# Kernel optimization log

Hardware: AMD Instinct MI355X
Metric: run time of the kernel (lower is better)

## Reference

```python
import jax, jax.numpy as jnp
import numpy as np

B, S, H, E, V, T = 512, 140, 512, 256, 1000, 21  # T = day_walk_max + 1
PAD, SOS = 0, 2
NDAYS, DLEN = 7, 20


def setup_inputs() -> dict:
    key = jax.random.key(0)
    ks = jax.random.split(key, 16)
    s = 0.05
    return {
        "encoder_hidden": jax.random.normal(ks[0], (1, B, H), jnp.float32),
        "encoder_outputs": jax.random.normal(ks[1], (B, S, H), jnp.float32),
        "label": jax.random.randint(ks[2], (B, T + 1), 0, V),
        "numpairs": jax.random.randint(ks[3], (B, S), 0, 10),
        "emb": jax.random.normal(ks[4], (V, E), jnp.float32) * s,
        "W_ih": jax.random.normal(ks[5], (3 * H, E), jnp.float32) * s,
        "W_hh": jax.random.normal(ks[6], (3 * H, H), jnp.float32) * s,
        "b_ih": jnp.zeros((3 * H,), jnp.float32),
        "b_hh": jnp.zeros((3 * H,), jnp.float32),
        "attn_Wa": jax.random.normal(ks[7], (H, H), jnp.float32) * s,
        "wa_W": jax.random.normal(ks[8], (H, 2 * H), jnp.float32) * s,
        "fc_W": jax.random.normal(ks[9], (V, H), jnp.float32) * s,
        "fc_b": jnp.zeros((V,), jnp.float32),
    }


def _decode(encoder_hidden, encoder_outputs, label, numpairs,
            emb, W_ih, W_hh, b_ih, b_hh, attn_Wa, wa_W, fc_W, fc_b):
    # Luong 'general' attention over 7 day-segments of 20 steps each.
    enc_days = encoder_outputs.reshape(B, NDAYS, DLEN, H)
    mask_day = numpairs.reshape(B, NDAYS, DLEN) != PAD
    # energy is hidden-independent: precompute once  [B,7,20,H]
    energy_day = jnp.einsum('bdsh,gh->bdsg', enc_days, attn_Wa)

    def step(carry, lab_t):
        dec_in, h = carry  # dec_in [B] int, h [B,H]
        # per-day additive attention with numpair padding mask
        sc = jnp.einsum('bh,bdsh->bds', h, energy_day)
        sc = jnp.where(mask_day, sc, jnp.float32(-1e9))
        wd = jax.nn.softmax(sc, axis=-1)
        week = jnp.einsum('bds,bdsh->bdh', wd, enc_days)  # [B,7,H]
        # GRU cell (PyTorch gate layout r,z,n); dropout is identity at eval
        x = emb[dec_in]  # [B,E]
        gi = x @ W_ih.T + b_ih
        gh = h @ W_hh.T + b_hh
        i_r, i_z, i_n = jnp.split(gi, 3, axis=-1)
        h_r, h_z, h_n = jnp.split(gh, 3, axis=-1)
        r = jax.nn.sigmoid(i_r + h_r)
        z = jax.nn.sigmoid(i_z + h_z)
        n = jnp.tanh(i_n + r * h_n)
        h_new = (1.0 - z) * n + z * h  # [B,H]
        # week-level attention over the 7 day contexts (no mask)
        ew = jnp.einsum('bdh,gh->bdg', week, attn_Wa)
        aw = jax.nn.softmax(jnp.einsum('bh,bdh->bd', h_new, ew), axis=-1)
        ctx = jnp.einsum('bd,bdh->bh', aw, week)
        concat = jnp.concatenate([h_new, ctx], axis=-1)  # [B,2H]
        out = jax.nn.log_softmax(jnp.tanh(concat @ wa_W.T) @ fc_W.T + fc_b, axis=-1)
        return (lab_t, h_new), out  # teacher forcing: next input = label[:, t]

    dec0 = jnp.full((B,), SOS, dtype=label.dtype)
    h0 = encoder_hidden[0]  # [B,H]
    labels_t = label[:, :T].T  # [T,B]
    (last_in, _), outs = jax.lax.scan(step, (dec0, h0), labels_t)
    decoder_outputs = jnp.transpose(outs, (1, 0, 2))  # [B,T,V]
    return decoder_outputs, last_in[:, None]


def reference(encoder_hidden, encoder_outputs, label, numpairs,
              emb, W_ih, W_hh, b_ih, b_hh, attn_Wa, wa_W, fc_W, fc_b):
    return _decode(encoder_hidden, encoder_outputs, label, numpairs,
                   emb, W_ih, W_hh, b_ih, b_hh, attn_Wa, wa_W, fc_W, fc_b)
```

## Files before the change

kernel.cpp:

```cpp
#include <hip/hip_runtime.h>
#include <math.h>

typedef __attribute__((ext_vector_type(8))) short bf16x8;
typedef __attribute__((ext_vector_type(4))) float f32x4;

constexpr int NB = 512;
constexpr int NS = 140;
constexpr int NH = 512;
constexpr int NE = 256;
constexpr int NV = 1000;
constexpr int NVP = 1024;
constexpr int NT = 21;
constexpr int ND = 7;
constexpr int DL = 20;
constexpr int SOS = 2;
constexpr int LSTR = NT + 1;
constexpr int NROW = NT * NB;

__device__ __forceinline__ unsigned short f2bf(float f) {
  union { float f; unsigned u; } v; v.f = f;
  unsigned r = v.u + 0x7fffu + ((v.u >> 16) & 1u);
  return (unsigned short)(r >> 16);
}
__device__ __forceinline__ float bf2f(unsigned short h) {
  union { unsigned u; float f; } v; v.u = ((unsigned)h) << 16;
  return v.f;
}
__device__ __forceinline__ void unp8(uint4 v, float* o) {
  o[0] = bf2f((unsigned short)(v.x & 0xffffu)); o[1] = bf2f((unsigned short)(v.x >> 16));
  o[2] = bf2f((unsigned short)(v.y & 0xffffu)); o[3] = bf2f((unsigned short)(v.y >> 16));
  o[4] = bf2f((unsigned short)(v.z & 0xffffu)); o[5] = bf2f((unsigned short)(v.z >> 16));
  o[6] = bf2f((unsigned short)(v.w & 0xffffu)); o[7] = bf2f((unsigned short)(v.w >> 16));
}

template<int A16, int EPI, int OUT16>
__device__ __forceinline__ void gemm_body(
    const float* __restrict__ Af, const unsigned short* __restrict__ Ah,
    const unsigned short* __restrict__ Bt, const float* __restrict__ bias,
    float* __restrict__ C, unsigned short* __restrict__ C16,
    int K, int lda, int ldc, int bx, int by,
    unsigned short* As, unsigned short* Bs)
{
  const int tid = threadIdx.x;
  const int rowBase = by * 64, colBase = bx * 64;
  const int wave = tid >> 6, lane = tid & 63, quad = lane >> 4, l15 = lane & 15;
  const int rw = (wave & 1) * 32, cw = (wave >> 1) * 32;

  f32x4 acc[2][2];
#pragma unroll
  for (int i = 0; i < 2; ++i)
#pragma unroll
    for (int j = 0; j < 2; ++j)
#pragma unroll
      for (int r = 0; r < 4; ++r) acc[i][j][r] = 0.f;

  const int ar = tid >> 2;
  const int kq = (tid & 3) * 8;
  const float* aptrf = nullptr;
  const unsigned short* aptrh = nullptr;
  if (A16) aptrh = Ah + (size_t)(rowBase + ar) * lda + kq;
  else     aptrf = Af + (size_t)(rowBase + ar) * lda + kq;
  const unsigned short* bptr = Bt + (size_t)(colBase + ar) * K + kq;
  unsigned short* asd = &As[ar * 40 + kq];
  unsigned short* bsd = &Bs[ar * 40 + kq];

  float4 x0, x1;
  uint4 av;
  if (A16) {
    av = *(const uint4*)aptrh;
  } else {
    x0 = *(const float4*)aptrf; x1 = *(const float4*)(aptrf + 4);
  }
  uint4 bv = *(const uint4*)bptr;

  int cur = 0;
  for (int k0 = 0; k0 < K; k0 += 32) {
    uint4 aw;
    if (A16) {
      aw = av;
    } else {
      aw.x = (unsigned)f2bf(x0.x) | ((unsigned)f2bf(x0.y) << 16);
      aw.y = (unsigned)f2bf(x0.z) | ((unsigned)f2bf(x0.w) << 16);
      aw.z = (unsigned)f2bf(x1.x) | ((unsigned)f2bf(x1.y) << 16);
      aw.w = (unsigned)f2bf(x1.z) | ((unsigned)f2bf(x1.w) << 16);
    }
    *(uint4*)(asd + cur * 2560) = aw;
    *(uint4*)(bsd + cur * 2560) = bv;

    const int kn = k0 + 32;
    if (kn < K) {
      if (A16) {
        av = *(const uint4*)(aptrh + kn);
      } else {
        x0 = *(const float4*)(aptrf + kn);
        x1 = *(const float4*)(aptrf + kn + 4);
      }
      bv = *(const uint4*)(bptr + kn);
    }
    __syncthreads();

    const unsigned short* Ab = As + cur * 2560;
    const unsigned short* Bb = Bs + cur * 2560;
    const bf16x8 af0 = *(const bf16x8*)&Ab[(rw + l15) * 40 + quad * 8];
    const bf16x8 af1 = *(const bf16x8*)&Ab[(rw + 16 + l15) * 40 + quad * 8];
    const bf16x8 bf0 = *(const bf16x8*)&Bb[(cw + l15) * 40 + quad * 8];
    const bf16x8 bf1 = *(const bf16x8*)&Bb[(cw + 16 + l15) * 40 + quad * 8];
    acc[0][0] = __builtin_amdgcn_mfma_f32_16x16x32_bf16(af0, bf0, acc[0][0], 0, 0, 0);
    acc[0][1] = __builtin_amdgcn_mfma_f32_16x16x32_bf16(af0, bf1, acc[0][1], 0, 0, 0);
    acc[1][0] = __builtin_amdgcn_mfma_f32_16x16x32_bf16(af1, bf0, acc[1][0], 0, 0, 0);
    acc[1][1] = __builtin_amdgcn_mfma_f32_16x16x32_bf16(af1, bf1, acc[1][1], 0, 0, 0);
    cur ^= 1;
  }

#pragma unroll
  for (int i = 0; i < 2; ++i) {
    const int grow = rowBase + rw + 16 * i + quad * 4;
#pragma unroll
    for (int j = 0; j < 2; ++j) {
      const int gcol = colBase + cw + 16 * j + l15;
#pragma unroll
      for (int r = 0; r < 4; ++r) {
        float vo = acc[i][j][r];
        if (EPI == 1) vo += (gcol < NV) ? bias[gcol] : 0.f;
        if (EPI == 2) vo = tanhf(vo);
        if (OUT16) C16[(size_t)(grow + r) * ldc + gcol] = f2bf(vo);
        else       C[(size_t)(grow + r) * ldc + gcol] = vo;
      }
    }
  }
}

template<int A16, int EPI, int OUT16>
__global__ __launch_bounds__(256) void gemm_k(
    const float* __restrict__ Af, const unsigned short* __restrict__ Ah,
    const unsigned short* __restrict__ Bt, const float* __restrict__ bias,
    float* __restrict__ C, unsigned short* __restrict__ C16,
    int K, int lda, int ldc)
{
  __shared__ unsigned short As[2 * 64 * 40];
  __shared__ unsigned short Bs[2 * 64 * 40];
  gemm_body<A16, EPI, OUT16>(Af, Ah, Bt, bias, C, C16, K, lda, ldc,
                             blockIdx.x, blockIdx.y, As, Bs);
}

__global__ __launch_bounds__(256) void gemm_gather(
    const float* __restrict__ emb, const unsigned short* __restrict__ Wiht,
    unsigned short* __restrict__ Gi, const int* __restrict__ label)
{
  __shared__ unsigned short As[64 * 40];
  __shared__ unsigned short Bs[64 * 40];
  const int tid = threadIdx.x;
  const int rowBase = blockIdx.y * 64, colBase = blockIdx.x * 64;
  const int wave = tid >> 6, lane = tid & 63, quad = lane >> 4, l15 = lane & 15;
  const int rw = (wave & 1) * 32, cw = (wave >> 1) * 32;
  const int K = 256;

  f32x4 acc[2][2];
#pragma unroll
  for (int i = 0; i < 2; ++i)
#pragma unroll
    for (int j = 0; j < 2; ++j)
#pragma unroll
      for (int r = 0; r < 4; ++r) acc[i][j][r] = 0.f;

  const int ar = tid >> 2;
  const int kq = (tid & 3) * 8;
  const int aRowG = rowBase + ar;
  const int t = aRowG >> 9;
  const int b = aRowG & 511;
  const int dec = (t == 0) ? SOS : label[b * LSTR + (t - 1)];
  const float* aptr = emb + (size_t)dec * NE + kq;
  const unsigned short* bptr = Wiht + (size_t)(colBase + ar) * K + kq;
  unsigned short* asd = &As[ar * 40 + kq];
  unsigned short* bsd = &Bs[ar * 40 + kq];

  float4 x0 = *(const float4*)aptr;
  float4 x1 = *(const float4*)(aptr + 4);
  uint4 bv = *(const uint4*)bptr;

  for (int k0 = 0; k0 < K; k0 += 32) {
    uint4 aw;
    aw.x = (unsigned)f2bf(x0.x) | ((unsigned)f2bf(x0.y) << 16);
    aw.y = (unsigned)f2bf(x0.z) | ((unsigned)f2bf(x0.w) << 16);
    aw.z = (unsigned)f2bf(x1.x) | ((unsigned)f2bf(x1.y) << 16);
    aw.w = (unsigned)f2bf(x1.z) | ((unsigned)f2bf(x1.w) << 16);
    *(uint4*)asd = aw;
    *(uint4*)bsd = bv;
    __syncthreads();
    const int kn = k0 + 32;
    if (kn < K) {
      x0 = *(const float4*)(aptr + kn);
      x1 = *(const float4*)(aptr + kn + 4);
      bv = *(const uint4*)(bptr + kn);
    }
    const bf16x8 af0 = *(const bf16x8*)&As[(rw + l15) * 40 + quad * 8];
    const bf16x8 af1 = *(const bf16x8*)&As[(rw + 16 + l15) * 40 + quad * 8];
    const bf16x8 bf0 = *(const bf16x8*)&Bs[(cw + l15) * 40 + quad * 8];
    const bf16x8 bf1 = *(const bf16x8*)&Bs[(cw + 16 + l15) * 40 + quad * 8];
    acc[0][0] = __builtin_amdgcn_mfma_f32_16x16x32_bf16(af0, bf0, acc[0][0], 0, 0, 0);
    acc[0][1] = __builtin_amdgcn_mfma_f32_16x16x32_bf16(af0, bf1, acc[0][1], 0, 0, 0);
    acc[1][0] = __builtin_amdgcn_mfma_f32_16x16x32_bf16(af1, bf0, acc[1][0], 0, 0, 0);
    acc[1][1] = __builtin_amdgcn_mfma_f32_16x16x32_bf16(af1, bf1, acc[1][1], 0, 0, 0);
    __syncthreads();
  }

#pragma unroll
  for (int i = 0; i < 2; ++i) {
    const int grow = rowBase + rw + 16 * i + quad * 4;
#pragma unroll
    for (int j = 0; j < 2; ++j) {
      const int gcol = colBase + cw + 16 * j + l15;
#pragma unroll
      for (int r = 0; r < 4; ++r)
        Gi[(size_t)(grow + r) * 1536 + gcol] = f2bf(acc[i][j][r]);
    }
  }
}

__global__ __launch_bounds__(256) void step_fused(
    const float* __restrict__ Ht, const unsigned short* __restrict__ W1pk,
    const unsigned short* __restrict__ Gi_t,
    const float* __restrict__ b_ih, const float* __restrict__ b_hh,
    float* __restrict__ Hnext, float* __restrict__ Ut,
    unsigned short* __restrict__ U16t, int notLast)
{
  __shared__ __align__(16) char smem[46080];
  unsigned short* As = (unsigned short*)smem;
  unsigned short* Bs = (unsigned short*)(smem + 5120);
  float* Gbuf = (float*)smem;

  const int tid = threadIdx.x;
  const int wave = tid >> 6, lane = tid & 63, quad = lane >> 4, l15 = lane & 15;
  const int rowBase = blockIdx.y * 32;
  const int colBase = blockIdx.x * 256;

  f32x4 acc[2][4];
#pragma unroll
  for (int i = 0; i < 2; ++i)
#pragma unroll
    for (int j = 0; j < 4; ++j)
#pragma unroll
      for (int r = 0; r < 4; ++r) acc[i][j][r] = 0.f;

  const int ar = tid >> 3;
  const int kqa = (tid & 7) * 4;
  const float* aptr = Ht + (size_t)(rowBase + ar) * NH + kqa;
  const unsigned short* bbase = W1pk + (size_t)(colBase + tid) * 32;
  unsigned short* asd = As + ar * 40 + kqa;
  unsigned short* bsd = Bs + tid * 40;

  float4 xa = *(const float4*)aptr;
  uint4 bv0 = *(const uint4*)(bbase + 0);
  uint4 bv1 = *(const uint4*)(bbase + 8);
  uint4 bv2 = *(const uint4*)(bbase + 16);
  uint4 bv3 = *(const uint4*)(bbase + 24);

  int cur = 0;
  for (int k0 = 0; k0 < NH; k0 += 32) {
    ushort4 aw;
    aw.x = f2bf(xa.x); aw.y = f2bf(xa.y); aw.z = f2bf(xa.z); aw.w = f2bf(xa.w);
    *(ushort4*)(asd + cur * 1280) = aw;
    *(uint4*)(bsd + cur * 10240 + 0)  = bv0;
    *(uint4*)(bsd + cur * 10240 + 8)  = bv1;
    *(uint4*)(bsd + cur * 10240 + 16) = bv2;
    *(uint4*)(bsd + cur * 10240 + 24) = bv3;

    const int kn = k0 + 32;
    if (kn < NH) {
      xa = *(const float4*)(aptr + kn);
      const unsigned short* nb = bbase + (size_t)(kn >> 5) * (2048 * 32);
      bv0 = *(const uint4*)(nb + 0);
      bv1 = *(const uint4*)(nb + 8);
      bv2 = *(const uint4*)(nb + 16);
      bv3 = *(const uint4*)(nb + 24);
    }
    __syncthreads();

    const unsigned short* Ab = As + cur * 1280;
    const unsigned short* Bb = Bs + cur * 10240;
    const bf16x8 af0 = *(const bf16x8*)&Ab[(l15) * 40 + quad * 8];
    const bf16x8 af1 = *(const bf16x8*)&Ab[(16 + l15) * 40 + quad * 8];
#pragma unroll
    for (int j = 0; j < 4; ++j) {
      const bf16x8 bf = *(const bf16x8*)&Bb[(wave * 64 + j * 16 + l15) * 40 + quad * 8];
      acc[0][j] = __builtin_amdgcn_mfma_f32_16x16x32_bf16(af0, bf, acc[0][j], 0, 0, 0);
      acc[1][j] = __builtin_amdgcn_mfma_f32_16x16x32_bf16(af1, bf, acc[1][j], 0, 0, 0);
    }
    cur ^= 1;
  }
  __syncthreads();

#pragma unroll
  for (int i = 0; i < 2; ++i) {
#pragma unroll
    for (int j = 0; j < 4; ++j) {
#pragma unroll
      for (int r = 0; r < 4; ++r) {
        const int rl = 16 * i + quad * 4 + r;
        const int col = j * 16 + l15;
        if (wave == 3) {
          const float v = acc[i][j][r];
          const size_t off = (size_t)(rowBase + rl) * NH + blockIdx.x * 64 + col;
          Ut[off] = v;
          U16t[off] = f2bf(v);
        } else {
          Gbuf[(wave * 32 + rl) * 72 + col] = acc[i][j][r];
        }
      }
    }
  }
  __syncthreads();

  if (notLast) {
    const int rl = tid >> 3, c8 = (tid & 7) * 8;
    const int bg = rowBase + rl;
    const int jg = blockIdx.x * 64 + c8;
    const float* g0 = Gbuf + (0 * 32 + rl) * 72 + c8;
    const float* g1 = Gbuf + (1 * 32 + rl) * 72 + c8;
    const float* g2 = Gbuf + (2 * 32 + rl) * 72 + c8;
    const unsigned short* gp = Gi_t + (size_t)bg * 1536;
    float gr[8], gz[8], gn[8];
    { uint4 a = *(const uint4*)(gp + jg);        unp8(a, gr); }
    { uint4 a = *(const uint4*)(gp + 512 + jg);  unp8(a, gz); }
    { uint4 a = *(const uint4*)(gp + 1024 + jg); unp8(a, gn); }
    const float* hR = Ht + (size_t)bg * NH + jg;
    float* hW = Hnext + (size_t)bg * NH + jg;
    const float4 ho0 = *(const float4*)hR;
    const float4 ho1 = *(const float4*)(hR + 4);
    const float hov[8] = {ho0.x, ho0.y, ho0.z, ho0.w, ho1.x, ho1.y, ho1.z, ho1.w};
    float o[8];
#pragma unroll
    for (int c = 0; c < 8; ++c) {
      const int j = jg + c;
      const float ir  = gr[c] + b_ih[j];
      const float iz  = gz[c] + b_ih[512 + j];
      const float inn = gn[c] + b_ih[1024 + j];
      const float hr  = g0[c] + b_hh[j];
      const float hz  = g1[c] + b_hh[512 + j];
      const float hn  = g2[c] + b_hh[1024 + j];
      const float rg = 1.f / (1.f + expf(-(ir + hr)));
      const float zg = 1.f / (1.f + expf(-(iz + hz)));
      const float ng = tanhf(inn + rg * hn);
      o[c] = (1.f - zg) * ng + zg * hov[c];
    }
    *(float4*)hW = make_float4(o[0], o[1], o[2], o[3]);
    *(float4*)(hW + 4) = make_float4(o[4], o[5], o[6], o[7]);
  }
}

__global__ __launch_bounds__(256) void day_attn_mfma(
    const float* __restrict__ enc, const int* __restrict__ numpairs,
    const unsigned short* __restrict__ U16, unsigned short* __restrict__ week)
{
  __shared__ unsigned short Erow[32 * 520];
  __shared__ unsigned short ETs[512 * 36];
  __shared__ float S_lds[32 * 33];
  __shared__ unsigned short P_lds[32 * 40];

  const int tid = threadIdx.x;
  const int wave = tid >> 6, lane = tid & 63;
  const int quad = lane >> 4, l15 = lane & 15;
  const int b = blockIdx.x / ND, d = blockIdx.x % ND;
  const int mt = wave >> 1, nt = wave & 1;

  for (int i = tid; i < 512 * 6; i += 256)
    *(unsigned*)&ETs[(i / 6) * 36 + 20 + (i % 6) * 2] = 0;
  for (int i = tid; i < 640; i += 256) ((unsigned*)P_lds)[i] = 0;

  const float* eb = enc + ((size_t)b * NS + d * DL) * NH;
  for (int f = tid; f < DL * NH / 4; f += 256) {
    const int s = f >> 7, h = (f & 127) * 4;
    const float4 v = *(const float4*)(eb + s * NH + h);
    ushort4 hs;
    hs.x = f2bf(v.x); hs.y = f2bf(v.y); hs.z = f2bf(v.z); hs.w = f2bf(v.w);
    *(ushort4*)&Erow[s * 520 + h] = hs;
  }

  bf16x8 qa[16];
  {
    const int m = mt * 16 + l15;
    const int t = (m < NT + 1) ? m : NT;
    const unsigned short* qp = U16 + ((size_t)t * NB + b) * NH + quad * 8;
#pragma unroll
    for (int ks = 0; ks < 16; ++ks)
      qa[ks] = *(const bf16x8*)(qp + ks * 32);
  }
  __syncthreads();

  for (int i = tid; i < 64 * DL; i += 256) {
    const int s = i % DL, h8 = i / DL;
    const uint4 v = *(const uint4*)&Erow[s * 520 + h8 * 8];
    const unsigned short* u = (const unsigned short*)&v;
#pragma unroll
    for (int c = 0; c < 8; ++c)
      ETs[(h8 * 8 + c) * 36 + s] = u[c];
  }

  f32x4 sacc = {0.f, 0.f, 0.f, 0.f};
#pragma unroll
  for (int ks = 0; ks < 16; ++ks) {
    const bf16x8 bf = *(const bf16x8*)&Erow[(nt * 16 + l15) * 520 + ks * 32 + quad * 8];
    sacc = __builtin_amdgcn_mfma_f32_16x16x32_bf16(qa[ks], bf, sacc, 0, 0, 0);
  }
#pragma unroll
  for (int r = 0; r < 4; ++r)
    S_lds[(mt * 16 + quad * 4 + r) * 33 + nt * 16 + l15] = sacc[r];
  __syncthreads();

  {
    const int r = tid >> 3, c = tid & 7;
    const int base = b * NS + d * DL;
    float v0 = S_lds[r * 33 + c];
    if (numpairs[base + c] == 0) v0 = -1e9f;
    float v1 = S_lds[r * 33 + c + 8];
    if (numpairs[base + c + 8] == 0) v1 = -1e9f;
    float v2 = -1e30f;
    if (c < 4) {
      v2 = S_lds[r * 33 + c + 16];
      if (numpairs[base + c + 16] == 0) v2 = -1e9f;
    }
    float mx = fmaxf(fmaxf(v0, v1), v2);
    mx = fmaxf(mx, __shfl_xor(mx, 1));
    mx = fmaxf(mx, __shfl_xor(mx, 2));
    mx = fmaxf(mx, __shfl_xor(mx, 4));
    const float e0 = expf(v0 - mx), e1 = expf(v1 - mx);
    const float e2 = (c < 4) ? expf(v2 - mx) : 0.f;
    float sm = e0 + e1 + e2;
    sm += __shfl_xor(sm, 1);
    sm += __shfl_xor(sm, 2);
    sm += __shfl_xor(sm, 4);
    const float inv = 1.f / sm;
    P_lds[r * 40 + c] = f2bf(e0 * inv);
    P_lds[r * 40 + c + 8] = f2bf(e1 * inv);
    if (c < 4) P_lds[r * 40 + c + 16] = f2bf(e2 * inv);
  }
  __syncthreads();

  const bf16x8 pa = *(const bf16x8*)&P_lds[(mt * 16 + l15) * 40 + quad * 8];
#pragma unroll
  for (int j = 0; j < 16; ++j) {
    const int hcol = nt * 256 + j * 16;
    const bf16x8 bf = *(const bf16x8*)&ETs[(hcol + l15) * 36 + quad * 8];
    f32x4 oacc = {0.f, 0.f, 0.f, 0.f};
    oacc = __builtin_amdgcn_mfma_f32_16x16x32_bf16(pa, bf, oacc, 0, 0, 0);
#pragma unroll
    for (int r = 0; r < 4; ++r) {
      const int t = mt * 16 + quad * 4 + r;
      if (t < NT)
        week[(((size_t)t * NB + b) * ND + d) * NH + hcol + l15] = f2bf(oacc[r]);
    }
  }
}

__global__ __launch_bounds__(256) void wk_ctx(
    const float* __restrict__ U, const unsigned short* __restrict__ week,
    const float* __restrict__ H, unsigned short* __restrict__ concat)
{
  __shared__ float scS[16 * ND];
  __shared__ float awS[16 * ND];
  const int tid = threadIdx.x;
  const int t = blockIdx.x >> 5;
  const int grp = blockIdx.x & 31;
  const int b16 = tid >> 4, k16 = tid & 15;
  const int b = grp * 16 + b16;
  const float* vp = U + ((size_t)(t + 1) * NB + b) * NH + k16 * 32;
  const size_t wrow = ((size_t)t * NB + b) * ND;

  for (int d = 0; d < ND; ++d) {
    const unsigned short* wp = week + (wrow + d) * NH + k16 * 32;
    float p = 0.f;
#pragma unroll
    for (int q = 0; q < 8; ++q) {
      const float4 a = *(const float4*)(vp + q * 4);
      const ushort4 wv = *(const ushort4*)(wp + q * 4);
      p += a.x * bf2f(wv.x) + a.y * bf2f(wv.y) + a.z * bf2f(wv.z) + a.w * bf2f(wv.w);
    }
    p += __shfl_down(p, 8); p += __shfl_down(p, 4);
    p += __shfl_down(p, 2); p += __shfl_down(p, 1);
    if (k16 == 0) scS[b16 * ND + d] = p;
  }
  __syncthreads();
  if (tid < 16) {
    float s[ND], mx = -1e30f;
    for (int d = 0; d < ND; ++d) { s[d] = scS[tid * ND + d]; mx = fmaxf(mx, s[d]); }
    float sum = 0.f;
    for (int d = 0; d < ND; ++d) { float e = expf(s[d] - mx); s[d] = e; sum += e; }
    const float inv = 1.f / sum;
    for (int d = 0; d < ND; ++d) awS[tid * ND + d] = s[d] * inv;
  }
  __syncthreads();

  const int c0 = k16 * 32;
  const float* hp = H + ((size_t)(t + 1) * NB + b) * NH + c0;
  float aw[ND];
#pragma unroll
  for (int d = 0; d < ND; ++d) aw[d] = awS[b16 * ND + d];
  unsigned short* crow = concat + ((size_t)t * NB + b) * 1024;
#pragma unroll
  for (int q = 0; q < 8; ++q) {
    const int c = c0 + q * 4;
    const float4 hv = *(const float4*)(hp + q * 4);
    ushort4 hs;
    hs.x = f2bf(hv.x); hs.y = f2bf(hv.y); hs.z = f2bf(hv.z); hs.w = f2bf(hv.w);
    *(ushort4*)(crow + c) = hs;
    float4 cv = make_float4(0.f, 0.f, 0.f, 0.f);
#pragma unroll
    for (int d = 0; d < ND; ++d) {
      const ushort4 wv = *(const ushort4*)(week + (wrow + d) * NH + c);
      cv.x += aw[d] * bf2f(wv.x); cv.y += aw[d] * bf2f(wv.y);
      cv.z += aw[d] * bf2f(wv.z); cv.w += aw[d] * bf2f(wv.w);
    }
    ushort4 cs;
    cs.x = f2bf(cv.x); cs.y = f2bf(cv.y); cs.z = f2bf(cv.z); cs.w = f2bf(cv.w);
    *(ushort4*)(crow + 512 + c) = cs;
  }
}

__global__ __launch_bounds__(256) void lsm_k(
    const float* __restrict__ logits, float* __restrict__ out)
{
  __shared__ float red[8];
  const int tid = threadIdx.x;
  const int wave = tid >> 6, lane = tid & 63;
  const int r = blockIdx.x;
  const int t = r >> 9, b = r & (NB - 1);
  const float* row = logits + (size_t)r * NVP;
  float v[4];
  float mx = -1e30f;
#pragma unroll
  for (int k = 0; k < 4; ++k) {
    const int c = tid + k * 256;
    v[k] = row[c];
    if (c < NV) mx = fmaxf(mx, v[k]);
  }
#pragma unroll
  for (int off = 32; off; off >>= 1) mx = fmaxf(mx, __shfl_xor(mx, off));
  if (lane == 0) red[wave] = mx;
  __syncthreads();
  mx = fmaxf(fmaxf(red[0], red[1]), fmaxf(red[2], red[3]));
  float s = 0.f;
#pragma unroll
  for (int k = 0; k < 4; ++k) {
    const int c = tid + k * 256;
    if (c < NV) s += expf(v[k] - mx);
  }
#pragma unroll
  for (int off = 32; off; off >>= 1) s += __shfl_xor(s, off);
  if (lane == 0) red[4 + wave] = s;
  __syncthreads();
  const float lse = mx + logf(red[4] + red[5] + red[6] + red[7]);
  float* orow = out + ((size_t)b * NT + t) * NV;
#pragma unroll
  for (int k = 0; k < 4; ++k) {
    const int c = tid + k * 256;
    if (c < NV) orow[c] = v[k] - lse;
  }
}

__global__ void write_last(const int* __restrict__ label, float* __restrict__ out2)
{
  const int b = blockIdx.x * 256 + threadIdx.x;
  if (b < NB) out2[b] = (float)label[b * LSTR + (NT - 1)];
}

__global__ __launch_bounds__(256) void pack_w1pk(
    const float* __restrict__ Whh, const float* __restrict__ Wa,
    unsigned short* __restrict__ W1pk)
{
  const int idx = blockIdx.x * 256 + threadIdx.x;
  const int np = idx >> 9, k = idx & 511;
  const int g = np >> 8, rem = np & 255, gate = rem >> 6, j = g * 64 + (rem & 63);
  float v;
  if (gate < 3) v = Whh[(size_t)(gate * 512 + j) * 512 + k];
  else          v = Wa[(size_t)k * 512 + j];
  W1pk[((size_t)(k >> 5) * 2048 + np) * 32 + (k & 31)] = f2bf(v);
}

__global__ __launch_bounds__(256) void cast4(
    const float4* __restrict__ in, ushort4* __restrict__ out, int n4)
{
  const int i = blockIdx.x * 256 + threadIdx.x;
  if (i < n4) {
    const float4 x = in[i];
    ushort4 r;
    r.x = f2bf(x.x); r.y = f2bf(x.y); r.z = f2bf(x.z); r.w = f2bf(x.w);
    out[i] = r;
  }
}

extern "C" void kernel_launch(void* const* d_in, const int* in_sizes, int n_in,
                              void* d_out, int out_size, void* d_ws, size_t ws_size,
                              hipStream_t stream)
{
  const float* enc_h  = (const float*)d_in[0];
  const float* enc    = (const float*)d_in[1];
  const int*   label  = (const int*)d_in[2];
  const int*   numprs = (const int*)d_in[3];
  const float* emb    = (const float*)d_in[4];
  const float* W_ih   = (const float*)d_in[5];
  const float* W_hh   = (const float*)d_in[6];
  const float* b_ih   = (const float*)d_in[7];
  const float* b_hh   = (const float*)d_in[8];
  const float* Wa     = (const float*)d_in[9];
  const float* wa_W   = (const float*)d_in[10];
  const float* fc_W   = (const float*)d_in[11];
  const float* fc_b   = (const float*)d_in[12];
  float* out = (float*)d_out;

  float* f = (float*)d_ws;
  float* H_all   = f; f += (size_t)(NT + 1) * NB * NH;
  float* U_all   = f; f += (size_t)(NT + 1) * NB * NH;
  float* logitsW = f; f += (size_t)NROW * NVP;
  unsigned short* us = (unsigned short*)f;
  unsigned short* U16    = us; us += (size_t)(NT + 1) * NB * NH;
  unsigned short* W1pk   = us; us += (size_t)2048 * 512;
  unsigned short* W3t    = us; us += (size_t)512 * 1024;
  unsigned short* W4t    = us; us += (size_t)NVP * 512;
  unsigned short* Wiht   = us; us += (size_t)1536 * 256;
  unsigned short* Gi     = us; us += (size_t)NT * NB * 1536;
  unsigned short* week   = us; us += (size_t)NT * NB * ND * NH;
  unsigned short* concatW= us; us += (size_t)NROW * 1024;
  unsigned short* aBuf   = us; us += (size_t)NROW * 512;

  const dim3 blk(256);
  const size_t BH = (size_t)NB * NH;

  hipMemcpyAsync(H_all, enc_h, BH * sizeof(float),
                 hipMemcpyDeviceToDevice, stream);

  pack_w1pk<<<dim3(2048 * 512 / 256), blk, 0, stream>>>(W_hh, Wa, W1pk);
  cast4<<<dim3(512 * 1024 / 4 / 256), blk, 0, stream>>>(
      (const float4*)wa_W, (ushort4*)W3t, 512 * 1024 / 4);
  cast4<<<dim3((NV * 512 / 4 + 255) / 256), blk, 0, stream>>>(
      (const float4*)fc_W, (ushort4*)W4t, NV * 512 / 4);
  hipMemsetAsync(W4t + (size_t)NV * 512, 0, (size_t)(NVP - NV) * 512 * 2, stream);
  cast4<<<dim3(1536 * 256 / 4 / 256), blk, 0, stream>>>(
      (const float4*)W_ih, (ushort4*)Wiht, 1536 * 256 / 4);
  gemm_gather<<<dim3(24, NT * 8), blk, 0, stream>>>(emb, Wiht, Gi, label);

  for (int t = 0; t <= NT; ++t) {
    const int notLast = (t < NT) ? 1 : 0;
    const int tg = (t < NT) ? t : NT - 1;
    step_fused<<<dim3(8, 16), blk, 0, stream>>>(
        H_all + (size_t)t * BH, W1pk, Gi + (size_t)tg * NB * 1536,
        b_ih, b_hh,
        H_all + (size_t)(notLast ? t + 1 : t) * BH,
        U_all + (size_t)t * BH, U16 + (size_t)t * BH, notLast);
  }

  day_attn_mfma<<<dim3(NB * ND), blk, 0, stream>>>(enc, numprs, U16, week);
  wk_ctx<<<dim3(NT * 32), blk, 0, stream>>>(U_all, week, H_all, concatW);
  gemm_k<1, 2, 1><<<dim3(8, NROW / 64), blk, 0, stream>>>(
      nullptr, concatW, W3t, nullptr, nullptr, aBuf, 1024, 1024, 512);
  gemm_k<1, 1, 0><<<dim3(16, NROW / 64), blk, 0, stream>>>(
      nullptr, aBuf, W4t, fc_b, logitsW, nullptr, 512, 512, NVP);
  lsm_k<<<dim3(NROW), blk, 0, stream>>>(logitsW, out);
  write_last<<<dim3(2), blk, 0, stream>>>(label, out + (size_t)NB * NT * NV);
}
```

Before: 784.8 us.

## Halve step kernel column tile to double grid, shrink day-attention LDS

The per-timestep fused GRU/U kernel now handles 32 hidden columns per block instead of 64, doubling the grid from 128 to 256 blocks and halving per-block LDS and accumulators. The weight packing is changed to match the new gate grouping. Separately, the day-attention kernel transposes the encoder tile in two halves so its transposed buffer needs half the LDS, which should allow more resident blocks at the cost of an extra barrier and a second transpose pass. Each step block now reloads A (hidden state) tiles for fewer output columns, so A traffic doubles.

New measurement: 675.0 us. 14.0% less time.

```diff
diff --git a/kernel.cpp b/kernel.cpp
--- a/kernel.cpp
+++ b/kernel.cpp
@@ -31,6 +31,10 @@
   o[2] = bf2f((unsigned short)(v.y & 0xffffu)); o[3] = bf2f((unsigned short)(v.y >> 16));
   o[4] = bf2f((unsigned short)(v.z & 0xffffu)); o[5] = bf2f((unsigned short)(v.z >> 16));
   o[6] = bf2f((unsigned short)(v.w & 0xffffu)); o[7] = bf2f((unsigned short)(v.w >> 16));
+}
+__device__ __forceinline__ void unp4(uint2 v, float* o) {
+  o[0] = bf2f((unsigned short)(v.x & 0xffffu)); o[1] = bf2f((unsigned short)(v.x >> 16));
+  o[2] = bf2f((unsigned short)(v.y & 0xffffu)); o[3] = bf2f((unsigned short)(v.y >> 16));
 }
 
 template<int A16, int EPI, int OUT16>
@@ -218,13 +222,13 @@
 }
 
 __global__ __launch_bounds__(256) void step_fused(
-    const float* __restrict__ Ht, const unsigned short* __restrict__ W1pk,
+    const float* __restrict__ Ht, const unsigned short* __restrict__ W2,
     const unsigned short* __restrict__ Gi_t,
     const float* __restrict__ b_ih, const float* __restrict__ b_hh,
     float* __restrict__ Hnext, float* __restrict__ Ut,
     unsigned short* __restrict__ U16t, int notLast)
 {
-  __shared__ __align__(16) char smem[46080];
+  __shared__ __align__(16) char smem[25600];
   unsigned short* As = (unsigned short*)smem;
   unsigned short* Bs = (unsigned short*)(smem + 5120);
   float* Gbuf = (float*)smem;
@@ -232,57 +236,51 @@
   const int tid = threadIdx.x;
   const int wave = tid >> 6, lane = tid & 63, quad = lane >> 4, l15 = lane & 15;
   const int rowBase = blockIdx.y * 32;
-  const int colBase = blockIdx.x * 256;
-
-  f32x4 acc[2][4];
+  const int G = blockIdx.x;
+
+  f32x4 acc[2][2];
 #pragma unroll
   for (int i = 0; i < 2; ++i)
 #pragma unroll
-    for (int j = 0; j < 4; ++j)
+    for (int j = 0; j < 2; ++j)
 #pragma unroll
       for (int r = 0; r < 4; ++r) acc[i][j][r] = 0.f;
 
   const int ar = tid >> 3;
   const int kqa = (tid & 7) * 4;
   const float* aptr = Ht + (size_t)(rowBase + ar) * NH + kqa;
-  const unsigned short* bbase = W1pk + (size_t)(colBase + tid) * 32;
+  const unsigned short* bsrc = W2 + (size_t)(G * 128) * 32 + (tid >> 1) * 32 + (tid & 1) * 16;
   unsigned short* asd = As + ar * 40 + kqa;
-  unsigned short* bsd = Bs + tid * 40;
+  unsigned short* bdst = Bs + (tid >> 1) * 40 + (tid & 1) * 16;
 
   float4 xa = *(const float4*)aptr;
-  uint4 bv0 = *(const uint4*)(bbase + 0);
-  uint4 bv1 = *(const uint4*)(bbase + 8);
-  uint4 bv2 = *(const uint4*)(bbase + 16);
-  uint4 bv3 = *(const uint4*)(bbase + 24);
+  uint4 b0 = ((const uint4*)bsrc)[0];
+  uint4 b1 = ((const uint4*)bsrc)[1];
 
   int cur = 0;
-  for (int k0 = 0; k0 < NH; k0 += 32) {
+  for (int c = 0; c < 16; ++c) {
     ushort4 aw;
     aw.x = f2bf(xa.x); aw.y = f2bf(xa.y); aw.z = f2bf(xa.z); aw.w = f2bf(xa.w);
     *(ushort4*)(asd + cur * 1280) = aw;
-    *(uint4*)(bsd + cur * 10240 + 0)  = bv0;
-    *(uint4*)(bsd + cur * 10240 + 8)  = bv1;
-    *(uint4*)(bsd + cur * 10240 + 16) = bv2;
-    *(uint4*)(bsd + cur * 10240 + 24) = bv3;
-
-    const int kn = k0 + 32;
-    if (kn < NH) {
-      xa = *(const float4*)(aptr + kn);
-      const unsigned short* nb = bbase + (size_t)(kn >> 5) * (2048 * 32);
-      bv0 = *(const uint4*)(nb + 0);
-      bv1 = *(const uint4*)(nb + 8);
-      bv2 = *(const uint4*)(nb + 16);
-      bv3 = *(const uint4*)(nb + 24);
+    *(uint4*)(bdst + cur * 5120) = b0;
+    *(uint4*)(bdst + cur * 5120 + 8) = b1;
+
+    const int cn = c + 1;
+    if (cn < 16) {
+      xa = *(const float4*)(aptr + cn * 32);
+      const unsigned short* nb = bsrc + (size_t)cn * (2048 * 32);
+      b0 = ((const uint4*)nb)[0];
+      b1 = ((const uint4*)nb)[1];
     }
     __syncthreads();
 
     const unsigned short* Ab = As + cur * 1280;
-    const unsigned short* Bb = Bs + cur * 10240;
+    const unsigned short* Bb = Bs + cur * 5120;
     const bf16x8 af0 = *(const bf16x8*)&Ab[(l15) * 40 + quad * 8];
     const bf16x8 af1 = *(const bf16x8*)&Ab[(16 + l15) * 40 + quad * 8];
 #pragma unroll
-    for (int j = 0; j < 4; ++j) {
-      const bf16x8 bf = *(const bf16x8*)&Bb[(wave * 64 + j * 16 + l15) * 40 + quad * 8];
+    for (int j = 0; j < 2; ++j) {
+      const bf16x8 bf = *(const bf16x8*)&Bb[(wave * 32 + j * 16 + l15) * 40 + quad * 8];
       acc[0][j] = __builtin_amdgcn_mfma_f32_16x16x32_bf16(af0, bf, acc[0][j], 0, 0, 0);
       acc[1][j] = __builtin_amdgcn_mfma_f32_16x16x32_bf16(af1, bf, acc[1][j], 0, 0, 0);
     }
@@ -293,18 +291,18 @@
 #pragma unroll
   for (int i = 0; i < 2; ++i) {
 #pragma unroll
-    for (int j = 0; j < 4; ++j) {
+    for (int j = 0; j < 2; ++j) {
 #pragma unroll
       for (int r = 0; r < 4; ++r) {
         const int rl = 16 * i + quad * 4 + r;
-        const int col = j * 16 + l15;
+        const int jj = j * 16 + l15;
+        const float v = acc[i][j][r];
         if (wave == 3) {
-          const float v = acc[i][j][r];
-          const size_t off = (size_t)(rowBase + rl) * NH + blockIdx.x * 64 + col;
+          const size_t off = (size_t)(rowBase + rl) * NH + G * 32 + jj;
           Ut[off] = v;
           U16t[off] = f2bf(v);
         } else {
-          Gbuf[(wave * 32 + rl) * 72 + col] = acc[i][j][r];
+          Gbuf[(wave * 32 + rl) * 40 + jj] = v;
         }
       }
     }
@@ -312,39 +310,43 @@
   __syncthreads();
 
   if (notLast) {
-    const int rl = tid >> 3, c8 = (tid & 7) * 8;
+    const int rl = tid >> 3, c4 = (tid & 7) * 4;
     const int bg = rowBase + rl;
-    const int jg = blockIdx.x * 64 + c8;
-    const float* g0 = Gbuf + (0 * 32 + rl) * 72 + c8;
-    const float* g1 = Gbuf + (1 * 32 + rl) * 72 + c8;
-    const float* g2 = Gbuf + (2 * 32 + rl) * 72 + c8;
+    const int j0 = G * 32 + c4;
+    const float4 g0 = *(const float4*)(Gbuf + (0 * 32 + rl) * 40 + c4);
+    const float4 g1 = *(const float4*)(Gbuf + (1 * 32 + rl) * 40 + c4);
+    const float4 g2 = *(const float4*)(Gbuf + (2 * 32 + rl) * 40 + c4);
     const unsigned short* gp = Gi_t + (size_t)bg * 1536;
-    float gr[8], gz[8], gn[8];
-    { uint4 a = *(const uint4*)(gp + jg);        unp8(a, gr); }
-    { uint4 a = *(const uint4*)(gp + 512 + jg);  unp8(a, gz); }
-    { uint4 a = *(const uint4*)(gp + 1024 + jg); unp8(a, gn); }
-    const float* hR = Ht + (size_t)bg * NH + jg;
-    float* hW = Hnext + (size_t)bg * NH + jg;
-    const float4 ho0 = *(const float4*)hR;
-    const float4 ho1 = *(const float4*)(hR + 4);
-    const float hov[8] = {ho0.x, ho0.y, ho0.z, ho0.w, ho1.x, ho1.y, ho1.z, ho1.w};
-    float o[8];
-#pragma unroll
-    for (int c = 0; c < 8; ++c) {
-      const int j = jg + c;
-      const float ir  = gr[c] + b_ih[j];
-      const float iz  = gz[c] + b_ih[512 + j];
-      const float inn = gn[c] + b_ih[1024 + j];
-      const float hr  = g0[c] + b_hh[j];
-      const float hz  = g1[c] + b_hh[512 + j];
-      const float hn  = g2[c] + b_hh[1024 + j];
-      const float rg = 1.f / (1.f + expf(-(ir + hr)));
-      const float zg = 1.f / (1.f + expf(-(iz + hz)));
-      const float ng = tanhf(inn + rg * hn);
+    float gr[4], gz[4], gn[4];
+    { uint2 a = *(const uint2*)(gp + j0);        unp4(a, gr); }
+    { uint2 a = *(const uint2*)(gp + 512 + j0);  unp4(a, gz); }
+    { uint2 a = *(const uint2*)(gp + 1024 + j0); unp4(a, gn); }
+    const float4 bi0 = *(const float4*)(b_ih + j0);
+    const float4 bi1 = *(const float4*)(b_ih + 512 + j0);
+    const float4 bi2 = *(const float4*)(b_ih + 1024 + j0);
+    const float4 bh0 = *(const float4*)(b_hh + j0);
+    const float4 bh1 = *(const float4*)(b_hh + 512 + j0);
+    const float4 bh2 = *(const float4*)(b_hh + 1024 + j0);
+    const float4 ho = *(const float4*)(Ht + (size_t)bg * NH + j0);
+    const float ghr[4] = {g0.x, g0.y, g0.z, g0.w};
+    const float ghz[4] = {g1.x, g1.y, g1.z, g1.w};
+    const float ghn[4] = {g2.x, g2.y, g2.z, g2.w};
+    const float bi0a[4] = {bi0.x, bi0.y, bi0.z, bi0.w};
+    const float bi1a[4] = {bi1.x, bi1.y, bi1.z, bi1.w};
+    const float bi2a[4] = {bi2.x, bi2.y, bi2.z, bi2.w};
+    const float bh0a[4] = {bh0.x, bh0.y, bh0.z, bh0.w};
+    const float bh1a[4] = {bh1.x, bh1.y, bh1.z, bh1.w};
+    const float bh2a[4] = {bh2.x, bh2.y, bh2.z, bh2.w};
+    const float hov[4] = {ho.x, ho.y, ho.z, ho.w};
+    float o[4];
+#pragma unroll
+    for (int c = 0; c < 4; ++c) {
+      const float rg = 1.f / (1.f + expf(-(gr[c] + bi0a[c] + ghr[c] + bh0a[c])));
+      const float zg = 1.f / (1.f + expf(-(gz[c] + bi1a[c] + ghz[c] + bh1a[c])));
+      const float ng = tanhf(gn[c] + bi2a[c] + rg * (ghn[c] + bh2a[c]));
       o[c] = (1.f - zg) * ng + zg * hov[c];
     }
-    *(float4*)hW = make_float4(o[0], o[1], o[2], o[3]);
-    *(float4*)(hW + 4) = make_float4(o[4], o[5], o[6], o[7]);
+    *(float4*)(Hnext + (size_t)bg * NH + j0) = make_float4(o[0], o[1], o[2], o[3]);
   }
 }
 
@@ -352,10 +354,11 @@
     const float* __restrict__ enc, const int* __restrict__ numpairs,
     const unsigned short* __restrict__ U16, unsigned short* __restrict__ week)
 {
-  __shared__ unsigned short Erow[32 * 520];
-  __shared__ unsigned short ETs[512 * 36];
-  __shared__ float S_lds[32 * 33];
-  __shared__ unsigned short P_lds[32 * 40];
+  __shared__ __align__(16) char smem[46016];
+  unsigned short* Erow = (unsigned short*)smem;
+  unsigned short* ETs  = (unsigned short*)(smem + 20800);
+  float*          S_lds = (float*)(smem + 39232);
+  unsigned short* P_lds = (unsigned short*)(smem + 43456);
 
   const int tid = threadIdx.x;
   const int wave = tid >> 6, lane = tid & 63;
@@ -363,7 +366,7 @@
   const int b = blockIdx.x / ND, d = blockIdx.x % ND;
   const int mt = wave >> 1, nt = wave & 1;
 
-  for (int i = tid; i < 512 * 6; i += 256)
+  for (int i = tid; i < 256 * 6; i += 256)
     *(unsigned*)&ETs[(i / 6) * 36 + 20 + (i % 6) * 2] = 0;
   for (int i = tid; i < 640; i += 256) ((unsigned*)P_lds)[i] = 0;
 
@@ -387,7 +390,7 @@
   }
   __syncthreads();
 
-  for (int i = tid; i < 64 * DL; i += 256) {
+  for (int i = tid; i < 32 * DL; i += 256) {
     const int s = i % DL, h8 = i / DL;
     const uint4 v = *(const uint4*)&Erow[s * 520 + h8 * 8];
     const unsigned short* u = (const unsigned short*)&v;
@@ -438,17 +441,32 @@
 
   const bf16x8 pa = *(const bf16x8*)&P_lds[(mt * 16 + l15) * 40 + quad * 8];
 #pragma unroll
-  for (int j = 0; j < 16; ++j) {
-    const int hcol = nt * 256 + j * 16;
-    const bf16x8 bf = *(const bf16x8*)&ETs[(hcol + l15) * 36 + quad * 8];
-    f32x4 oacc = {0.f, 0.f, 0.f, 0.f};
-    oacc = __builtin_amdgcn_mfma_f32_16x16x32_bf16(pa, bf, oacc, 0, 0, 0);
-#pragma unroll
-    for (int r = 0; r < 4; ++r) {
-      const int t = mt * 16 + quad * 4 + r;
-      if (t < NT)
-        week[(((size_t)t * NB + b) * ND + d) * NH + hcol + l15] = f2bf(oacc[r]);
-    }
+  for (int p = 0; p < 2; ++p) {
+    if (p == 1) {
+      for (int i = tid; i < 32 * DL; i += 256) {
+        const int s = i % DL, h8 = i / DL;
+        const uint4 v = *(const uint4*)&Erow[s * 520 + 256 + h8 * 8];
+        const unsigned short* u = (const unsigned short*)&v;
+#pragma unroll
+        for (int c = 0; c < 8; ++c)
+          ETs[(h8 * 8 + c) * 36 + s] = u[c];
+      }
+      __syncthreads();
+    }
+#pragma unroll
+    for (int j = 0; j < 8; ++j) {
+      const int hl = nt * 128 + j * 16;
+      const bf16x8 bf = *(const bf16x8*)&ETs[(hl + l15) * 36 + quad * 8];
+      f32x4 oacc = {0.f, 0.f, 0.f, 0.f};
+      oacc = __builtin_amdgcn_mfma_f32_16x16x32_bf16(pa, bf, oacc, 0, 0, 0);
+#pragma unroll
+      for (int r = 0; r < 4; ++r) {
+        const int t = mt * 16 + quad * 4 + r;
+        if (t < NT)
+          week[(((size_t)t * NB + b) * ND + d) * NH + p * 256 + hl + l15] = f2bf(oacc[r]);
+      }
+    }
+    if (p == 0) __syncthreads();
   }
 }
 
@@ -563,17 +581,17 @@
   if (b < NB) out2[b] = (float)label[b * LSTR + (NT - 1)];
 }
 
-__global__ __launch_bounds__(256) void pack_w1pk(
+__global__ __launch_bounds__(256) void pack_w2(
     const float* __restrict__ Whh, const float* __restrict__ Wa,
-    unsigned short* __restrict__ W1pk)
+    unsigned short* __restrict__ W2)
 {
   const int idx = blockIdx.x * 256 + threadIdx.x;
   const int np = idx >> 9, k = idx & 511;
-  const int g = np >> 8, rem = np & 255, gate = rem >> 6, j = g * 64 + (rem & 63);
+  const int G = np >> 7, rem = np & 127, gate = rem >> 5, j = G * 32 + (rem & 31);
   float v;
   if (gate < 3) v = Whh[(size_t)(gate * 512 + j) * 512 + k];
   else          v = Wa[(size_t)k * 512 + j];
-  W1pk[((size_t)(k >> 5) * 2048 + np) * 32 + (k & 31)] = f2bf(v);
+  W2[((size_t)(k >> 5) * 2048 + np) * 32 + (k & 31)] = f2bf(v);
 }
 
 __global__ __launch_bounds__(256) void cast4(
@@ -613,7 +631,7 @@
   float* logitsW = f; f += (size_t)NROW * NVP;
   unsigned short* us = (unsigned short*)f;
   unsigned short* U16    = us; us += (size_t)(NT + 1) * NB * NH;
-  unsigned short* W1pk   = us; us += (size_t)2048 * 512;
+  unsigned short* W2     = us; us += (size_t)2048 * 512;
   unsigned short* W3t    = us; us += (size_t)512 * 1024;
   unsigned short* W4t    = us; us += (size_t)NVP * 512;
   unsigned short* Wiht   = us; us += (size_t)1536 * 256;
@@ -628,7 +646,7 @@
   hipMemcpyAsync(H_all, enc_h, BH * sizeof(float),
                  hipMemcpyDeviceToDevice, stream);
 
-  pack_w1pk<<<dim3(2048 * 512 / 256), blk, 0, stream>>>(W_hh, Wa, W1pk);
+  pack_w2<<<dim3(2048 * 512 / 256), blk, 0, stream>>>(W_hh, Wa, W2);
   cast4<<<dim3(512 * 1024 / 4 / 256), blk, 0, stream>>>(
       (const float4*)wa_W, (ushort4*)W3t, 512 * 1024 / 4);
   cast4<<<dim3((NV * 512 / 4 + 255) / 256), blk, 0, stream>>>(
@@ -641,8 +659,8 @@
   for (int t = 0; t <= NT; ++t) {
     const int notLast = (t < NT) ? 1 : 0;
     const int tg = (t < NT) ? t : NT - 1;
-    step_fused<<<dim3(8, 16), blk, 0, stream>>>(
-        H_all + (size_t)t * BH, W1pk, Gi + (size_t)tg * NB * 1536,
+    step_fused<<<dim3(16, 16), blk, 0, stream>>>(
+        H_all + (size_t)t * BH, W2, Gi + (size_t)tg * NB * 1536,
         b_ih, b_hh,
         H_all + (size_t)(notLast ? t + 1 : t) * BH,
         U_all + (size_t)t * BH, U16 + (size_t)t * BH, notLast);
```
